# Optimization experiments

Measured on AMD Instinct MI355X. Metric: run time of the kernel, lower is better.

The kernel has to match this reference:

```python
import jax, jax.numpy as jnp
import numpy as np

B, S, HID, H, DK = 16, 1024, 512, 8, 64
NEG = -1e30


def setup_inputs() -> dict:
    key = jax.random.key(0)
    kx, kl, kq, kk, kv, ko = jax.random.split(key, 6)
    x = jax.random.normal(kx, (B, S, HID), dtype=jnp.float32)
    # mask is a prefix of ones per sample (the torch code fills nmask[i, :nsum, :nsum])
    lengths = jax.random.randint(kl, (B,), S // 2, S + 1)
    mask = (jnp.arange(S)[None, :] < lengths[:, None]).astype(jnp.int32)
    scale = 0.02
    Wq = jax.random.normal(kq, (H, HID, DK), dtype=jnp.float32) * scale  # stacked per-head Linear weights
    Wk = jax.random.normal(kk, (H, HID, DK), dtype=jnp.float32) * scale
    Wv = jax.random.normal(kv, (H, HID, DK), dtype=jnp.float32) * scale
    Wout = jax.random.normal(ko, (H * DK, HID), dtype=jnp.float32) * scale
    return {"x": x, "mask": mask, "Wq": Wq, "Wk": Wk, "Wv": Wv, "Wout": Wout}


def reference(x, mask, Wq, Wk, Wv, Wout):
    # x: [B,S,HID], mask: [B,S] int prefix mask
    nsum = mask.sum(-1).astype(jnp.float32)          # [B]
    valid = mask.astype(bool)                         # [B,S]
    pair = valid[:, :, None] & valid[:, None, :]      # [B,S,S] == nmask from the torch loop
    # batched per-head projections (equivalent to the per-head Linear loop)
    Q = jnp.einsum('bsh,nhd->bnsd', x, Wq)            # [B,H,S,DK]
    K = jnp.einsum('bsh,nhd->bnsd', x, Wk)
    V = jnp.einsum('bsh,nhd->bnsd', x, Wv)
    scores = jnp.einsum('bnqd,bnkd->bnqk', Q, K)      # [B,H,S,S]
    scores = scores / jnp.sqrt(nsum)[:, None, None, None]  # per-sample sqrt(len) scale
    scores = jnp.where(pair[:, None, :, :], scores, NEG)   # masked_softmax: -1e30 at masked slots
    p = jax.nn.softmax(scores, axis=-1)
    attn = jnp.einsum('bnqk,bnkd->bnqd', p, V)        # [B,H,S,DK]
    h = attn.transpose(0, 2, 1, 3).reshape(B, S, H * DK)  # concat heads along feature dim
    return jnp.einsum('bsf,fh->bsh', h, Wout)         # W_out, no bias
```

## Files before the change

### kernel.cpp

```cpp
#include <hip/hip_runtime.h>
#include <math.h>

constexpr int CB = 16;
constexpr int CS = 1024;
constexpr int CHID = 512;
constexpr int CH = 8;
constexpr int CDK = 64;

typedef _Float16 f16;
typedef __attribute__((ext_vector_type(8))) _Float16 f16x8;
typedef __attribute__((ext_vector_type(4))) _Float16 f16x4;
typedef __attribute__((ext_vector_type(4))) float f32x4;
typedef __attribute__((ext_vector_type(4))) unsigned int u32x4;
typedef __attribute__((ext_vector_type(2))) unsigned int u32x2;

__device__ inline f32x4 mfma16(f16x8 a, f16x8 b, f32x4 c) {
  return __builtin_amdgcn_mfma_f32_16x16x32_f16(a, b, c, 0, 0, 0);
}

__device__ inline void gld16(const void* g, void* l) {
  __builtin_amdgcn_global_load_lds(
      (const __attribute__((address_space(1))) void*)g,
      (__attribute__((address_space(3))) void*)l, 16, 0, 0);
}

__device__ inline float fast_exp2(float x) {
#if __has_builtin(__builtin_amdgcn_exp2f)
  return __builtin_amdgcn_exp2f(x);
#else
  return __expf(x * 0.6931471805599453f);
#endif
}

__device__ inline unsigned pack_rne(float a, float b) {
  union { f16 h[2]; unsigned u; } c;
  c.h[0] = (f16)a;
  c.h[1] = (f16)b;
  return c.u;
}

__device__ inline void quad_transpose(unsigned& x, unsigned& y) {
#if __has_builtin(__builtin_amdgcn_permlane32_swap) && \
    __has_builtin(__builtin_amdgcn_permlane16_swap)
  u32x2 a = __builtin_amdgcn_permlane32_swap(x, y, false, false);
  u32x2 b = __builtin_amdgcn_permlane16_swap(a[0], a[1], false, false);
  x = b[0];
  y = b[1];
#else
  asm volatile(
      "s_nop 1\n\t"
      "v_permlane32_swap_b32 %0, %1\n\t"
      "s_nop 1\n\t"
      "v_permlane16_swap_b32 %0, %1\n\t"
      "s_nop 1"
      : "+v"(x), "+v"(y));
#endif
}

#define LOG2E 1.4426950408889634f

__global__ __launch_bounds__(256) void prep_kernel(const float4* __restrict__ x,
                                                   f16x4* __restrict__ xh,
                                                   const int* __restrict__ mask,
                                                   int* __restrict__ lens,
                                                   float* __restrict__ Vsum) {
  const int bid = blockIdx.x, t = threadIdx.x;
  __shared__ int red[256];
  if (bid < 8192) {
    const int idx = bid * 256 + t;
    const float4 v = x[idx];
    f16x4 o;
    o[0] = (f16)v.x; o[1] = (f16)v.y; o[2] = (f16)v.z; o[3] = (f16)v.w;
    xh[idx] = o;
  } else {
    const int b = bid - 8192;
    const int g = b * 256 + t;
    Vsum[g * 2] = 0.f;
    Vsum[g * 2 + 1] = 0.f;
    int s = 0;
    for (int i = t; i < CS; i += 256) s += mask[b * CS + i];
    red[t] = s;
    __syncthreads();
    for (int off = 128; off > 0; off >>= 1) {
      if (t < off) red[t] += red[t + off];
      __syncthreads();
    }
    if (t == 0) lens[b] = red[0];
  }
}

__global__ __launch_bounds__(256) void cast_w_kernel(const float* __restrict__ Wq,
                                                     const float* __restrict__ Wk,
                                                     const float* __restrict__ Wv,
                                                     const float* __restrict__ Wout,
                                                     f16* __restrict__ wtAll) {
  const int y = blockIdx.y, kb = blockIdx.x, t = threadIdx.x;
  const int k0 = kb * 64;
  const float* src;
  int ldsrc;
  f16* dst;
  if (y < 24) {
    const int which = y >> 3, h = y & 7;
    const float* W = (which == 0) ? Wq : (which == 1) ? Wk : Wv;
    src = W + (size_t)h * 32768 + (size_t)k0 * 64;
    ldsrc = 64;
    dst = wtAll + (size_t)which * 262144 + (size_t)h * 32768;
  } else {
    const int c = y - 24;
    src = Wout + (size_t)k0 * 512 + c * 64;
    ldsrc = 512;
    dst = wtAll + (size_t)3 * 262144 + (size_t)c * 64 * 512;
  }

  __shared__ float Ts[64][68];
  {
    const int kr = t >> 4, cg = (t & 15) * 4;
#pragma unroll
    for (int rr = 0; rr < 4; ++rr) {
      const float4 v = *(const float4*)&src[(size_t)(rr * 16 + kr) * ldsrc + cg];
      Ts[rr * 16 + kr][cg] = v.x;
      Ts[rr * 16 + kr][cg + 1] = v.y;
      Ts[rr * 16 + kr][cg + 2] = v.z;
      Ts[rr * 16 + kr][cg + 3] = v.w;
    }
  }
  __syncthreads();
  {
    const int n = t >> 2, seg = t & 3;
    f16x8 a, b;
#pragma unroll
    for (int j = 0; j < 8; ++j) {
      a[j] = (f16)Ts[seg * 16 + j][n];
      b[j] = (f16)Ts[seg * 16 + 8 + j][n];
    }
    f16* d = &dst[(size_t)n * 512 + k0 + seg * 16];
    *(f16x8*)d = a;
    *(f16x8*)(d + 8) = b;
  }
}

__global__ __launch_bounds__(256) void qkvf_kernel(
    const f16* __restrict__ xh, const f16* __restrict__ wtAll,
    const int* __restrict__ lens, f16* __restrict__ Qh, f16* __restrict__ Kh,
    f16* __restrict__ Vth, float* __restrict__ Vsum) {
  const int ct = blockIdx.x, rt = blockIdx.y;
  const int which = ct >> 2, hp = ct & 3;
  const f16* Wt = wtAll + (size_t)which * 262144 + (size_t)hp * 65536;
  const int row0 = rt * 128;
  const int b = row0 >> 10, s0 = row0 & 1023;
  const int h0 = hp * 2;
  const int t = threadIdx.x;
  const int w = t >> 6, lane = t & 63, quad = lane >> 4, lcol = lane & 15;
  const int wr = w >> 1, wc = w & 1;

  __shared__ union SM {
    struct { f16 Xs[128][64]; f16 Ws[128][64]; } a;
    f16 Ts[128][136];
  } sm;

  f32x4 acc[4][4];
#pragma unroll
  for (int i = 0; i < 4; ++i)
#pragma unroll
    for (int j = 0; j < 4; ++j) acc[i][j] = (f32x4){0.f, 0.f, 0.f, 0.f};

  for (int k0 = 0; k0 < CHID; k0 += 64) {
    __syncthreads();
#pragma unroll
    for (int i = 0; i < 4; ++i) {
      const int c = t + 256 * i, r = c >> 3, sg = c & 7;
      const int gsw = (sg ^ (r & 7)) * 8;
      gld16(&xh[(size_t)(row0 + r) * CHID + k0 + gsw],
            (char*)&sm.a.Xs[0][0] + c * 16);
      gld16(&Wt[(size_t)r * CHID + k0 + gsw], (char*)&sm.a.Ws[0][0] + c * 16);
    }
    __syncthreads();

    f16x8 bf0[4], bf1[4];
#pragma unroll
    for (int j = 0; j < 4; ++j) {
      const int br = wc * 64 + j * 16 + lcol;
      bf0[j] = *(const f16x8*)&sm.a.Ws[br][(quad ^ (br & 7)) * 8];
      bf1[j] = *(const f16x8*)&sm.a.Ws[br][((quad ^ 4) ^ (br & 7)) * 8];
    }
#pragma unroll
    for (int i = 0; i < 4; ++i) {
      const int ar = wr * 64 + i * 16 + lcol;
      const f16x8 af0 = *(const f16x8*)&sm.a.Xs[ar][(quad ^ (ar & 7)) * 8];
      const f16x8 af1 =
          *(const f16x8*)&sm.a.Xs[ar][((quad ^ 4) ^ (ar & 7)) * 8];
#pragma unroll
      for (int j = 0; j < 4; ++j) {
        acc[i][j] = mfma16(af0, bf0[j], acc[i][j]);
        acc[i][j] = mfma16(af1, bf1[j], acc[i][j]);
      }
    }
  }

  if (which == 2) {
#pragma unroll
    for (int j = 0; j < 4; ++j) {
      float ps = 0.f;
#pragma unroll
      for (int i = 0; i < 4; ++i)
#pragma unroll
        for (int rr = 0; rr < 4; ++rr) ps += acc[i][j][rr];
      ps += __shfl_xor(ps, 16);
      ps += __shfl_xor(ps, 32);
      if (quad == 0) {
        const int d128 = wc * 64 + j * 16 + lcol;
        const int h = h0 + (d128 >> 6), d = d128 & 63;
        atomicAdd(&Vsum[((size_t)b * CH + h) * CDK + d], ps);
      }
    }
    __syncthreads();
#pragma unroll
    for (int i = 0; i < 4; ++i)
#pragma unroll
      for (int j = 0; j < 4; ++j) {
        f16x4 v4;
#pragma unroll
        for (int rr = 0; rr < 4; ++rr) v4[rr] = (f16)acc[i][j][rr];
        *(f16x4*)&sm.Ts[wc * 64 + j * 16 + lcol][wr * 64 + i * 16 + quad * 4] =
            v4;
      }
    __syncthreads();
    const int c16 = t & 15;
#pragma unroll
    for (int p = 0; p < 8; ++p) {
      const int vr = p * 16 + (t >> 4);
      const int h = h0 + (vr >> 6), d = vr & 63;
      *(f16x8*)&Vth[(((size_t)b * CH + h) * CDK + d) * CS + s0 + c16 * 8] =
          *(const f16x8*)&sm.Ts[vr][c16 * 8];
    }
  } else {
    const float qsc = (which == 0) ? rsqrtf((float)lens[b]) * LOG2E : 1.0f;
    __syncthreads();
#pragma unroll
    for (int i = 0; i < 4; ++i)
#pragma unroll
      for (int j = 0; j < 4; ++j)
#pragma unroll
        for (int rr = 0; rr < 4; ++rr)
          sm.Ts[wr * 64 + i * 16 + quad * 4 + rr][wc * 64 + j * 16 + lcol] =
              (f16)(acc[i][j][rr] * qsc);
    __syncthreads();
    f16* O = (which == 0) ? Qh : Kh;
    const int c8 = t & 7;
#pragma unroll
    for (int p = 0; p < 4; ++p) {
      const int row = p * 32 + (t >> 3);
#pragma unroll
      for (int half = 0; half < 2; ++half) {
        const int h = h0 + half;
        *(f16x8*)&O[(((size_t)b * CH + h) * CS + s0 + row) * CDK + c8 * 8] =
            *(const f16x8*)&sm.Ts[row][half * 64 + c8 * 8];
      }
    }
  }
}

__global__ __launch_bounds__(256, 4) void attn_kernel(
    const f16* __restrict__ Qh, const f16* __restrict__ Kh,
    const f16* __restrict__ Vth, const int* __restrict__ lens,
    const float* __restrict__ Vsum, f16* __restrict__ Hbh) {
  const int qt = blockIdx.x, h = blockIdx.y, b = blockIdx.z;
  const int n = lens[b];
  const int t = threadIdx.x, w = t >> 6, lane = t & 63, quad = lane >> 4,
            lcol = lane & 15;

  const size_t bh = ((size_t)b * CH + h) * CS;
  const size_t bhd = ((size_t)b * CH + h) * CDK;

  const int nt = (n + 63) >> 6;
  const int rem = n & 63;
  const int ntm = rem ? nt - 1 : nt;

  __shared__ union SM {
    struct { f16 Ks[2][64][72]; f16 Vs[2][64][72]; } kv;
    f16 St[4][32][72];
  } sm;

  const int qbase = qt * 128 + w * 32;
  f16x8 qa[2][2];
#pragma unroll
  for (int set = 0; set < 2; ++set) {
    const size_t qr = bh + qbase + set * 16 + lcol;
    qa[set][0] = *(const f16x8*)&Qh[qr * CDK + quad * 8];
    qa[set][1] = *(const f16x8*)&Qh[qr * CDK + 32 + quad * 8];
  }

  f16x8 vones;
#pragma unroll
  for (int j = 0; j < 8; ++j) vones[j] = (f16)1.0f;

  f32x4 o[2][4];
#pragma unroll
  for (int set = 0; set < 2; ++set)
#pragma unroll
    for (int dt = 0; dt < 4; ++dt) o[set][dt] = (f32x4){0.f, 0.f, 0.f, 0.f};
  f32x4 o_l[2] = {(f32x4){0.f, 0.f, 0.f, 0.f}, (f32x4){0.f, 0.f, 0.f, 0.f}};

  f16x8 pk[2], pv[2];
#pragma unroll
  for (int i = 0; i < 2; ++i) {
    const int c = t + 256 * i, r = c >> 3, sg = c & 7;
    pk[i] = *(const f16x8*)&Kh[(bh + r) * CDK + sg * 8];
    pv[i] = *(const f16x8*)&Vth[(bhd + r) * CS + sg * 8];
  }
#pragma unroll
  for (int i = 0; i < 2; ++i) {
    const int c = t + 256 * i, r = c >> 3, sg = c & 7;
    *(f16x8*)&sm.kv.Ks[0][r][sg * 8] = pk[i];
    *(f16x8*)&sm.kv.Vs[0][r][sg * 8] = pv[i];
  }
  __syncthreads();

  auto ktile = [&](const int kt, const bool masked) __attribute__((always_inline)) {
    const int cur = kt & 1, nxt = cur ^ 1;
    const int ktn = (kt + 1 < nt) ? kt + 1 : kt;
#pragma unroll
    for (int i = 0; i < 2; ++i) {
      const int c = t + 256 * i, r = c >> 3, sg = c & 7;
      pk[i] = *(const f16x8*)&Kh[(bh + ktn * 64 + r) * CDK + sg * 8];
      pv[i] = *(const f16x8*)&Vth[(bhd + r) * CS + ktn * 64 + sg * 8];
    }

    f16x8 pa[2][2];
#pragma unroll
    for (int set = 0; set < 2; ++set) {
      f32x4 st[4];
#pragma unroll
      for (int ct = 0; ct < 4; ++ct) {
        const f16x8 kb0 = *(const f16x8*)&sm.kv.Ks[cur][ct * 16 + lcol][quad * 8];
        const f16x8 kb1 =
            *(const f16x8*)&sm.kv.Ks[cur][ct * 16 + lcol][32 + quad * 8];
        st[ct] = mfma16(kb0, qa[set][0], (f32x4){0.f, 0.f, 0.f, 0.f});
        st[ct] = mfma16(kb1, qa[set][1], st[ct]);
      }
      unsigned pkd[4][2];
#pragma unroll
      for (int c = 0; c < 4; ++c) {
        float p[4];
#pragma unroll
        for (int r = 0; r < 4; ++r) {
          float e = fast_exp2(st[c][r]);
          if (masked) {
            const bool kvld = (kt * 64 + c * 16 + quad * 4 + r) < n;
            e = kvld ? e : 0.f;
          }
          p[r] = e;
        }
        pkd[c][0] = pack_rne(p[0], p[1]);
        pkd[c][1] = pack_rne(p[2], p[3]);
      }
#pragma unroll
      for (int half = 0; half < 2; ++half) {
        unsigned x0 = pkd[2 * half][0], y0 = pkd[2 * half + 1][0];
        unsigned x1 = pkd[2 * half][1], y1 = pkd[2 * half + 1][1];
        quad_transpose(x0, y0);
        quad_transpose(x1, y1);
        union { u32x4 u; f16x8 h; } cc;
        cc.u = (u32x4){x0, x1, y0, y1};
        pa[set][half] = cc.h;
      }
    }

#pragma unroll
    for (int dt = 0; dt < 4; ++dt) {
      const f16x8 vb0 = *(const f16x8*)&sm.kv.Vs[cur][dt * 16 + lcol][quad * 8];
      const f16x8 vb1 =
          *(const f16x8*)&sm.kv.Vs[cur][dt * 16 + lcol][32 + quad * 8];
#pragma unroll
      for (int set = 0; set < 2; ++set) {
        o[set][dt] = mfma16(pa[set][0], vb0, o[set][dt]);
        o[set][dt] = mfma16(pa[set][1], vb1, o[set][dt]);
      }
    }
#pragma unroll
    for (int set = 0; set < 2; ++set) {
      o_l[set] = mfma16(pa[set][0], vones, o_l[set]);
      o_l[set] = mfma16(pa[set][1], vones, o_l[set]);
    }

#pragma unroll
    for (int i = 0; i < 2; ++i) {
      const int c = t + 256 * i, r = c >> 3, sg = c & 7;
      *(f16x8*)&sm.kv.Ks[nxt][r][sg * 8] = pk[i];
      *(f16x8*)&sm.kv.Vs[nxt][r][sg * 8] = pv[i];
    }
    __syncthreads();
  };

  int kt = 0;
  for (; kt < ntm; ++kt) ktile(kt, false);
  if (rem) ktile(kt, true);

  float invl[2][4];
#pragma unroll
  for (int set = 0; set < 2; ++set)
#pragma unroll
    for (int r = 0; r < 4; ++r) invl[set][r] = 1.0f / o_l[set][r];

#pragma unroll
  for (int set = 0; set < 2; ++set)
#pragma unroll
    for (int dt = 0; dt < 4; ++dt)
#pragma unroll
      for (int r = 0; r < 4; ++r) {
        const int srow_l = set * 16 + quad * 4 + r;
        const int d = dt * 16 + lcol;
        const float val = (qbase + srow_l < n)
                              ? o[set][dt][r] * invl[set][r]
                              : Vsum[bhd + d] * (1.0f / 1024.0f);
        sm.St[w][srow_l][d] = (f16)val;
      }
  {
    const int lr = lane >> 3, lc = lane & 7;
#pragma unroll
    for (int p = 0; p < 4; ++p) {
      const int row = p * 8 + lr;
      *(f16x8*)&Hbh[((size_t)b * CS + qbase + row) * (CH * CDK) + h * CDK +
                    lc * 8] = *(const f16x8*)&sm.St[w][row][lc * 8];
    }
  }
}

__global__ __launch_bounds__(256) void outp_kernel(const f16* __restrict__ Hbh,
                                                   const f16* __restrict__ woutt,
                                                   float* __restrict__ out) {
  const int rt = blockIdx.x, ctile = blockIdx.y;
  const int row0 = rt * 128, col0 = ctile * 128;
  const f16* Wt = woutt + (size_t)col0 * CHID;
  const int t = threadIdx.x;
  const int w = t >> 6, lane = t & 63, quad = lane >> 4, lcol = lane & 15;
  const int wr = w >> 1, wc = w & 1;

  __shared__ f16 Hs[128][64];
  __shared__ f16 Ws[128][64];

  f32x4 acc[4][4];
#pragma unroll
  for (int i = 0; i < 4; ++i)
#pragma unroll
    for (int j = 0; j < 4; ++j) acc[i][j] = (f32x4){0.f, 0.f, 0.f, 0.f};

  for (int k0 = 0; k0 < CHID; k0 += 64) {
    __syncthreads();
#pragma unroll
    for (int i = 0; i < 4; ++i) {
      const int c = t + 256 * i, r = c >> 3, sg = c & 7;
      const int gsw = (sg ^ (r & 7)) * 8;
      gld16(&Hbh[(size_t)(row0 + r) * CHID + k0 + gsw],
            (char*)&Hs[0][0] + c * 16);
      gld16(&Wt[(size_t)r * CHID + k0 + gsw], (char*)&Ws[0][0] + c * 16);
    }
    __syncthreads();

    f16x8 bf0[4], bf1[4];
#pragma unroll
    for (int j = 0; j < 4; ++j) {
      const int br = wc * 64 + j * 16 + lcol;
      bf0[j] = *(const f16x8*)&Ws[br][(quad ^ (br & 7)) * 8];
      bf1[j] = *(const f16x8*)&Ws[br][((quad ^ 4) ^ (br & 7)) * 8];
    }
#pragma unroll
    for (int i = 0; i < 4; ++i) {
      const int ar = wr * 64 + i * 16 + lcol;
      const f16x8 af0 = *(const f16x8*)&Hs[ar][(quad ^ (ar & 7)) * 8];
      const f16x8 af1 = *(const f16x8*)&Hs[ar][((quad ^ 4) ^ (ar & 7)) * 8];
#pragma unroll
      for (int j = 0; j < 4; ++j) {
        acc[i][j] = mfma16(af0, bf0[j], acc[i][j]);
        acc[i][j] = mfma16(af1, bf1[j], acc[i][j]);
      }
    }
  }

#pragma unroll
  for (int i = 0; i < 4; ++i) {
#pragma unroll
    for (int rr = 0; rr < 4; ++rr) {
      const size_t rg = row0 + wr * 64 + i * 16 + quad * 4 + rr;
#pragma unroll
      for (int j = 0; j < 4; ++j)
        out[rg * CHID + col0 + wc * 64 + j * 16 + lcol] = acc[i][j][rr];
    }
  }
}

extern "C" void kernel_launch(void* const* d_in, const int* in_sizes, int n_in,
                              void* d_out, int out_size, void* d_ws,
                              size_t ws_size, hipStream_t stream) {
  const float* x = (const float*)d_in[0];
  const int* mask = (const int*)d_in[1];
  const float* Wq = (const float*)d_in[2];
  const float* Wk = (const float*)d_in[3];
  const float* Wv = (const float*)d_in[4];
  const float* Wout = (const float*)d_in[5];
  float* out = (float*)d_out;

  char* ws = (char*)d_ws;
  int* lens = (int*)ws;
  size_t off = 1024;
  const size_t NX = (size_t)CB * CS * CHID;
  const size_t NW = (size_t)CH * CHID * CDK;
  f16* xh = (f16*)(ws + off);    off += NX * 2;
  f16* wtAll = (f16*)(ws + off); off += NW * 4 * 2;
  f16* Qh = (f16*)(ws + off);    off += NX * 2;
  f16* Kh = (f16*)(ws + off);    off += NX * 2;
  f16* Vth = (f16*)(ws + off);   off += NX * 2;
  f16* Hbh = (f16*)(ws + off);   off += NX * 2;
  float* Vsum = (float*)(ws + off); off += (size_t)CB * CH * CDK * 4;
  f16* woutt = wtAll + NW * 3;

  prep_kernel<<<8208, 256, 0, stream>>>((const float4*)x, (f16x4*)xh, mask,
                                        lens, Vsum);
  cast_w_kernel<<<dim3(8, 32), 256, 0, stream>>>(Wq, Wk, Wv, Wout, wtAll);
  qkvf_kernel<<<dim3(12, 128), 256, 0, stream>>>(xh, wtAll, lens, Qh, Kh, Vth,
                                                 Vsum);
  attn_kernel<<<dim3(CS / 128, CH, CB), 256, 0, stream>>>(Qh, Kh, Vth, lens,
                                                          Vsum, Hbh);
  outp_kernel<<<dim3(128, 4), 256, 0, stream>>>(Hbh, woutt, out);
}
```

Baseline: 194.0 us.

## Enlarge attention blocks to 512 threads covering 256 queries with head-minor ordering

The attention kernel now runs 8 wavefronts per block, each still handling 32 query rows, so one block covers 256 queries. Each K/V tile staged in LDS is shared by twice as many queries, which halves per-query global K/V traffic, and each thread loads a single vector per tile. The grid is flattened so that the 8 heads of a (batch, query-tile) pair are adjacent in launch order. In exchange the block count drops to 512, and the larger score scratch plus barriers across 8 waves may limit occupancy and load balance given the variable sequence lengths.

```diff
diff --git a/kernel.cpp b/kernel.cpp
--- a/kernel.cpp
+++ b/kernel.cpp
@@ -260,11 +260,15 @@
   }
 }
 
-__global__ __launch_bounds__(256, 4) void attn_kernel(
+__global__ __launch_bounds__(512, 4) void attn_kernel(
     const f16* __restrict__ Qh, const f16* __restrict__ Kh,
     const f16* __restrict__ Vth, const int* __restrict__ lens,
     const float* __restrict__ Vsum, f16* __restrict__ Hbh) {
-  const int qt = blockIdx.x, h = blockIdx.y, b = blockIdx.z;
+  const int id = blockIdx.x;
+  const int h = id & 7;
+  const int slot = id >> 3;
+  const int qt = slot & 3;
+  const int b = slot >> 2;
   const int n = lens[b];
   const int t = threadIdx.x, w = t >> 6, lane = t & 63, quad = lane >> 4,
             lcol = lane & 15;
@@ -278,10 +282,10 @@
 
   __shared__ union SM {
     struct { f16 Ks[2][64][72]; f16 Vs[2][64][72]; } kv;
-    f16 St[4][32][72];
+    f16 St[8][32][72];
   } sm;
 
-  const int qbase = qt * 128 + w * 32;
+  const int qbase = qt * 256 + w * 32;
   f16x8 qa[2][2];
 #pragma unroll
   for (int set = 0; set < 2; ++set) {
@@ -301,30 +305,20 @@
     for (int dt = 0; dt < 4; ++dt) o[set][dt] = (f32x4){0.f, 0.f, 0.f, 0.f};
   f32x4 o_l[2] = {(f32x4){0.f, 0.f, 0.f, 0.f}, (f32x4){0.f, 0.f, 0.f, 0.f}};
 
-  f16x8 pk[2], pv[2];
-#pragma unroll
-  for (int i = 0; i < 2; ++i) {
-    const int c = t + 256 * i, r = c >> 3, sg = c & 7;
-    pk[i] = *(const f16x8*)&Kh[(bh + r) * CDK + sg * 8];
-    pv[i] = *(const f16x8*)&Vth[(bhd + r) * CS + sg * 8];
-  }
-#pragma unroll
-  for (int i = 0; i < 2; ++i) {
-    const int c = t + 256 * i, r = c >> 3, sg = c & 7;
-    *(f16x8*)&sm.kv.Ks[0][r][sg * 8] = pk[i];
-    *(f16x8*)&sm.kv.Vs[0][r][sg * 8] = pv[i];
-  }
+  const int sr = t >> 3, sg = t & 7;
+
+  f16x8 pk, pv;
+  pk = *(const f16x8*)&Kh[(bh + sr) * CDK + sg * 8];
+  pv = *(const f16x8*)&Vth[(bhd + sr) * CS + sg * 8];
+  *(f16x8*)&sm.kv.Ks[0][sr][sg * 8] = pk;
+  *(f16x8*)&sm.kv.Vs[0][sr][sg * 8] = pv;
   __syncthreads();
 
   auto ktile = [&](const int kt, const bool masked) __attribute__((always_inline)) {
     const int cur = kt & 1, nxt = cur ^ 1;
     const int ktn = (kt + 1 < nt) ? kt + 1 : kt;
-#pragma unroll
-    for (int i = 0; i < 2; ++i) {
-      const int c = t + 256 * i, r = c >> 3, sg = c & 7;
-      pk[i] = *(const f16x8*)&Kh[(bh + ktn * 64 + r) * CDK + sg * 8];
-      pv[i] = *(const f16x8*)&Vth[(bhd + r) * CS + ktn * 64 + sg * 8];
-    }
+    pk = *(const f16x8*)&Kh[(bh + ktn * 64 + sr) * CDK + sg * 8];
+    pv = *(const f16x8*)&Vth[(bhd + sr) * CS + ktn * 64 + sg * 8];
 
     f16x8 pa[2][2];
 #pragma unroll
@@ -383,12 +377,8 @@
       o_l[set] = mfma16(pa[set][1], vones, o_l[set]);
     }
 
-#pragma unroll
-    for (int i = 0; i < 2; ++i) {
-      const int c = t + 256 * i, r = c >> 3, sg = c & 7;
-      *(f16x8*)&sm.kv.Ks[nxt][r][sg * 8] = pk[i];
-      *(f16x8*)&sm.kv.Vs[nxt][r][sg * 8] = pv[i];
-    }
+    *(f16x8*)&sm.kv.Ks[nxt][sr][sg * 8] = pk;
+    *(f16x8*)&sm.kv.Vs[nxt][sr][sg * 8] = pv;
     __syncthreads();
   };
 
@@ -519,7 +509,6 @@
   cast_w_kernel<<<dim3(8, 32), 256, 0, stream>>>(Wq, Wk, Wv, Wout, wtAll);
   qkvf_kernel<<<dim3(12, 128), 256, 0, stream>>>(xh, wtAll, lens, Qh, Kh, Vth,
                                                  Vsum);
-  attn_kernel<<<dim3(CS / 128, CH, CB), 256, 0, stream>>>(Qh, Kh, Vth, lens,
-                                                          Vsum, Hbh);
+  attn_kernel<<<512, 512, 0, stream>>>(Qh, Kh, Vth, lens, Vsum, Hbh);
   outp_kernel<<<dim3(128, 4), 256, 0, stream>>>(Hbh, woutt, out);
 }
```

After: 192.4 us. No clear change (-0.8%).
